# Optimization experiments

Measured on AMD Instinct MI355X. Metric: run time of the kernel, lower is better.

Reference implementation:

```python
import jax, jax.numpy as jnp
import numpy as np

WS = 7          # window_size
NH = 12         # num_heads
EPS = 1e-5      # LayerNorm eps


def setup_inputs() -> dict:
    key = jax.random.key(0)
    ks = jax.random.split(key, 8)
    B, H, W, C = 32, 56, 56, 384
    x = jax.random.normal(ks[0], (B, H * W, C), dtype=jnp.float32)
    s = 1.0 / np.sqrt(C)
    return {
        "x": x,
        "ln_gamma": jnp.ones((C,), jnp.float32),
        "ln_beta": jnp.zeros((C,), jnp.float32),
        "w_in": jax.random.normal(ks[1], (3 * C, C), jnp.float32) * s,   # torch in_proj_weight
        "b_in": jnp.zeros((3 * C,), jnp.float32),
        "w_out": jax.random.normal(ks[2], (C, C), jnp.float32) * s,      # torch out_proj.weight
        "b_out": jnp.zeros((C,), jnp.float32),
        "H": H,
        "W": W,
    }


def reference(x, ln_gamma, ln_beta, w_in, b_in, w_out, b_out, H, W):
    B, N, C = x.shape
    assert N == H * W
    hd = C // NH
    shortcut = x

    # LayerNorm
    mu = jnp.mean(x, axis=-1, keepdims=True)
    var = jnp.mean((x - mu) ** 2, axis=-1, keepdims=True)
    y = (x - mu) * jax.lax.rsqrt(var + EPS) * ln_gamma + ln_beta

    # window partition (pads are static Python ints)
    y = y.reshape(B, H, W, C)
    pad_h = (WS - H % WS) % WS
    pad_w = (WS - W % WS) % WS
    y = jnp.pad(y, ((0, 0), (0, pad_h), (0, pad_w), (0, 0)))
    Hp, Wp = H + pad_h, W + pad_w
    nh, nw = Hp // WS, Wp // WS
    y = y.reshape(B, nh, WS, nw, WS, C).transpose(0, 1, 3, 2, 4, 5)
    y = y.reshape(B * nh * nw, WS * WS, C)   # [NWIN, L, C]

    # MHA (torch nn.MultiheadAttention, batch_first)
    qkv = y @ w_in.T + b_in                   # [NWIN, L, 3C]
    q, k, v = jnp.split(qkv, 3, axis=-1)
    NWIN, L, _ = y.shape
    q = q.reshape(NWIN, L, NH, hd).transpose(0, 2, 1, 3)
    k = k.reshape(NWIN, L, NH, hd).transpose(0, 2, 1, 3)
    v = v.reshape(NWIN, L, NH, hd).transpose(0, 2, 1, 3)
    scores = jnp.einsum("whqd,whkd->whqk", q, k) / jnp.sqrt(jnp.float32(hd))
    attn = jax.nn.softmax(scores, axis=-1)
    o = jnp.einsum("whqk,whkd->whqd", attn, v)
    o = o.transpose(0, 2, 1, 3).reshape(NWIN, L, C)
    o = o @ w_out.T + b_out

    # window reverse + unpad + residual
    o = o.reshape(B, nh, nw, WS, WS, C).transpose(0, 1, 3, 2, 4, 5)
    o = o.reshape(B, Hp, Wp, C)[:, :H, :W, :].reshape(B, N, C)
    return shortcut + o
```

## Files before the change

kernel.cpp:

```cpp
#include <hip/hip_runtime.h>

typedef __bf16 bf16x8 __attribute__((ext_vector_type(8)));
typedef float f32x4 __attribute__((ext_vector_type(4)));
typedef unsigned short ushort8 __attribute__((ext_vector_type(8)));
typedef unsigned int uu2 __attribute__((ext_vector_type(2)));

#define LDS_AS(p) ((__attribute__((address_space(3))) void*)(p))
#define GLB_AS(p) ((const __attribute__((address_space(1))) void*)(p))

__device__ __forceinline__ unsigned short f2bf(float f) {
    union { float f; unsigned u; } v; v.f = f;
    unsigned r = v.u + 0x7fffu + ((v.u >> 16) & 1u);
    return (unsigned short)(r >> 16);
}

__global__ __launch_bounds__(256) void convw_kernel(
    const float* __restrict__ wi, const float* __restrict__ wo,
    unsigned short* __restrict__ qw, unsigned short* __restrict__ ow)
{
    const int i = blockIdx.x * 256 + threadIdx.x;
    if (i < 1152 * 384) qw[i] = f2bf(wi[i]);
    if (i < 384 * 384)  ow[i] = f2bf(wo[i]);
}

__global__ __launch_bounds__(256) void ln_kernel(
    const float* __restrict__ x, const float* __restrict__ gam,
    const float* __restrict__ bet, unsigned short* __restrict__ y)
{
    const int lane = threadIdx.x & 63;
    const int wv   = threadIdx.x >> 6;
    const int m    = blockIdx.x * 4 + wv;
    const int win  = m / 49, l = m - win * 49;
    const int b = win >> 6, wh = (win >> 3) & 7, ww = win & 7;
    const int i = l / 7, j = l - i * 7;
    const float2* xr = (const float2*)(x + ((size_t)b * 3136 + (wh * 7 + i) * 56 + (ww * 7 + j)) * 384);

    float2 v[3];
    float s = 0.f, ss = 0.f;
#pragma unroll
    for (int t = 0; t < 3; ++t) {
        v[t] = xr[t * 64 + lane];
        s  += v[t].x + v[t].y;
        ss += v[t].x * v[t].x + v[t].y * v[t].y;
    }
#pragma unroll
    for (int d = 1; d < 64; d <<= 1) {
        s  += __shfl_xor(s, d, 64);
        ss += __shfl_xor(ss, d, 64);
    }
    const float mu  = s * (1.f / 384.f);
    const float var = ss * (1.f / 384.f) - mu * mu;
    const float rs  = rsqrtf(var + 1e-5f);

    unsigned* yr = (unsigned*)(y + (size_t)m * 384);
#pragma unroll
    for (int t = 0; t < 3; ++t) {
        const int c = (t * 64 + lane) * 2;
        float a0 = (v[t].x - mu) * rs * gam[c]     + bet[c];
        float a1 = (v[t].y - mu) * rs * gam[c + 1] + bet[c + 1];
        yr[t * 64 + lane] = (unsigned)f2bf(a0) | ((unsigned)f2bf(a1) << 16);
    }
}

template <int N_, int EPI>
__global__ __launch_bounds__(256) void gemm_kernel(
    const unsigned short* __restrict__ A,
    const unsigned short* __restrict__ Bw,
    const float* __restrict__ bias,
    unsigned short* __restrict__ obf,
    const float* __restrict__ xres,
    float* __restrict__ oflt)
{
    __shared__ unsigned short As[3][128 * 32];
    __shared__ unsigned short Bs[3][128 * 32];
    const int lane = threadIdx.x & 63;
    const int wv   = threadIdx.x >> 6;

    const int NB = N_ / 128;
    int sw = blockIdx.x;
    if ((gridDim.x & 7) == 0)
        sw = (sw & 7) * (int)(gridDim.x >> 3) + (sw >> 3);
    const int my = sw / NB;
    const int m0 = my * 128;
    const int n0 = (sw - my * NB) * 128;

    const int wm = (wv & 1) * 64;
    const int wn = (wv >> 1) * 64;
    const int cl = lane & 15;
    const int qd = lane >> 4;
    const int srow = wv * 16 + (lane >> 2);
    const int scol = ((lane & 3) ^ ((lane >> 3) & 3)) * 8;
    const int rc   = (qd ^ ((cl >> 1) & 3)) * 8;

    const unsigned short* gA = A  + (size_t)(m0 + srow) * 384 + scol;
    const unsigned short* gB = Bw + (size_t)(n0 + srow) * 384 + scol;

    f32x4 acc[4][4] = {};

#define STAGE(BUF, KB) do {                                                                                   \
    __builtin_amdgcn_global_load_lds(GLB_AS(gA + (KB) * 32),            LDS_AS(&As[BUF][(wv * 16) * 32]),      16, 0, 0); \
    __builtin_amdgcn_global_load_lds(GLB_AS(gA + 64 * 384 + (KB) * 32), LDS_AS(&As[BUF][(64 + wv * 16) * 32]), 16, 0, 0); \
    __builtin_amdgcn_global_load_lds(GLB_AS(gB + (KB) * 32),            LDS_AS(&Bs[BUF][(wv * 16) * 32]),      16, 0, 0); \
    __builtin_amdgcn_global_load_lds(GLB_AS(gB + 64 * 384 + (KB) * 32), LDS_AS(&Bs[BUF][(64 + wv * 16) * 32]), 16, 0, 0); \
  } while (0)

    STAGE(0, 0);
    STAGE(1, 1);

#pragma unroll
    for (int kb = 0; kb < 12; ++kb) {
        const int cur = kb % 3;
        if (kb < 11) asm volatile("s_waitcnt vmcnt(4)\n\ts_barrier" ::: "memory");
        else         asm volatile("s_waitcnt vmcnt(0)\n\ts_barrier" ::: "memory");

        if (kb < 10) STAGE((kb + 2) % 3, kb + 2);

        bf16x8 af[4], bfr[4];
#pragma unroll
        for (int mt = 0; mt < 4; ++mt)
            af[mt] = *(const bf16x8*)(&As[cur][(wm + mt * 16 + cl) * 32 + rc]);
#pragma unroll
        for (int nt = 0; nt < 4; ++nt)
            bfr[nt] = *(const bf16x8*)(&Bs[cur][(wn + nt * 16 + cl) * 32 + rc]);
#pragma unroll
        for (int mt = 0; mt < 4; ++mt)
#pragma unroll
            for (int nt = 0; nt < 4; ++nt)
                acc[mt][nt] = __builtin_amdgcn_mfma_f32_16x16x32_bf16(bfr[nt], af[mt], acc[mt][nt], 0, 0, 0);
    }
#undef STAGE

#pragma unroll
    for (int mt = 0; mt < 4; ++mt) {
        const int m = m0 + wm + mt * 16 + cl;
        size_t rowbase = 0;
        if (EPI == 1) {
            const int win = m / 49, l = m - win * 49;
            const int b = win >> 6, wh = (win >> 3) & 7, ww = win & 7;
            const int i = l / 7, j = l - i * 7;
            rowbase = ((size_t)b * 3136 + (wh * 7 + i) * 56 + (ww * 7 + j)) * 384;
        }
#pragma unroll
        for (int nt = 0; nt < 4; ++nt) {
            const int nb = n0 + wn + nt * 16 + qd * 4;
            const f32x4 bv = *(const f32x4*)(bias + nb);
            if (EPI == 0) {
                uu2 p;
                p[0] = (unsigned)f2bf(acc[mt][nt][0] + bv[0]) |
                       ((unsigned)f2bf(acc[mt][nt][1] + bv[1]) << 16);
                p[1] = (unsigned)f2bf(acc[mt][nt][2] + bv[2]) |
                       ((unsigned)f2bf(acc[mt][nt][3] + bv[3]) << 16);
                *(uu2*)(obf + (size_t)m * N_ + nb) = p;
            } else {
                const f32x4 xr = *(const f32x4*)(xres + rowbase + nb);
                f32x4 o;
#pragma unroll
                for (int r = 0; r < 4; ++r) o[r] = acc[mt][nt][r] + bv[r] + xr[r];
                *(f32x4*)(oflt + rowbase + nb) = o;
            }
        }
    }
}

__global__ __launch_bounds__(256) void attn_kernel(
    const unsigned short* __restrict__ qkv, unsigned short* __restrict__ o)
{
    __shared__ unsigned short P[4][64 * 72];
    const int lane = threadIdx.x & 63;
    const int wv   = threadIdx.x >> 6;
    const int cl = lane & 15;
    const int qd = lane >> 4;
    const int g   = blockIdx.x * 4 + wv;
    const int win = g / 12;
    const int h   = g - win * 12;
    const unsigned short* base = qkv + (size_t)win * (49 * 1152);

    bf16x8 aq[4], bk[4];
#pragma unroll
    for (int mt = 0; mt < 4; ++mt) {
        const int l = mt * 16 + cl;
        bf16x8 z = {};
        if (l < 49) z = *(const bf16x8*)(base + (size_t)l * 1152 + h * 32 + qd * 8);
        aq[mt] = z;
    }
#pragma unroll
    for (int nt = 0; nt < 4; ++nt) {
        const int lk = nt * 16 + cl;
        bf16x8 z = {};
        if (lk < 49) z = *(const bf16x8*)(base + (size_t)lk * 1152 + 384 + h * 32 + qd * 8);
        bk[nt] = z;
    }
    f32x4 s[4][4] = {};
#pragma unroll
    for (int mt = 0; mt < 4; ++mt)
#pragma unroll
        for (int nt = 0; nt < 4; ++nt)
            s[mt][nt] = __builtin_amdgcn_mfma_f32_16x16x32_bf16(aq[mt], bk[nt], s[mt][nt], 0, 0, 0);

    const float scale = 0.17677669529663687f;
#pragma unroll
    for (int mt = 0; mt < 4; ++mt)
#pragma unroll
        for (int nt = 0; nt < 4; ++nt)
#pragma unroll
            for (int r = 0; r < 4; ++r) {
                float t = s[mt][nt][r] * scale;
                if (nt * 16 + cl >= 49) t = -1e30f;
                s[mt][nt][r] = t;
            }

#pragma unroll
    for (int mt = 0; mt < 4; ++mt)
#pragma unroll
        for (int r = 0; r < 4; ++r) {
            float mx = fmaxf(fmaxf(s[mt][0][r], s[mt][1][r]), fmaxf(s[mt][2][r], s[mt][3][r]));
            mx = fmaxf(mx, __shfl_xor(mx, 1, 64));
            mx = fmaxf(mx, __shfl_xor(mx, 2, 64));
            mx = fmaxf(mx, __shfl_xor(mx, 4, 64));
            mx = fmaxf(mx, __shfl_xor(mx, 8, 64));
            float sm = 0.f;
#pragma unroll
            for (int nt = 0; nt < 4; ++nt) {
                const float p = __expf(s[mt][nt][r] - mx);
                s[mt][nt][r] = p;
                sm += p;
            }
            sm += __shfl_xor(sm, 1, 64);
            sm += __shfl_xor(sm, 2, 64);
            sm += __shfl_xor(sm, 4, 64);
            sm += __shfl_xor(sm, 8, 64);
            const float inv = 1.f / sm;
#pragma unroll
            for (int nt = 0; nt < 4; ++nt)
                s[mt][nt][r] *= inv;
        }

    unsigned short* Pw = &P[wv][0];
#pragma unroll
    for (int mt = 0; mt < 4; ++mt)
#pragma unroll
        for (int nt = 0; nt < 4; ++nt)
#pragma unroll
            for (int r = 0; r < 4; ++r)
                Pw[(mt * 16 + qd * 4 + r) * 72 + nt * 16 + cl] = f2bf(s[mt][nt][r]);

    f32x4 oa[4][2] = {};
    const unsigned short* vbase = base + 768 + h * 32;
#pragma unroll
    for (int kk = 0; kk < 2; ++kk) {
        bf16x8 ap[4];
#pragma unroll
        for (int mt = 0; mt < 4; ++mt)
            ap[mt] = *(const bf16x8*)(Pw + (mt * 16 + cl) * 72 + kk * 32 + qd * 8);
#pragma unroll
        for (int nt = 0; nt < 2; ++nt) {
            ushort8 tv;
#pragma unroll
            for (int jj = 0; jj < 8; ++jj) {
                const int lk = kk * 32 + qd * 8 + jj;
                tv[jj] = (lk < 49) ? vbase[(size_t)lk * 1152 + nt * 16 + cl] : (unsigned short)0;
            }
            const bf16x8 bv = __builtin_bit_cast(bf16x8, tv);
#pragma unroll
            for (int mt = 0; mt < 4; ++mt)
                oa[mt][nt] = __builtin_amdgcn_mfma_f32_16x16x32_bf16(ap[mt], bv, oa[mt][nt], 0, 0, 0);
        }
    }

    unsigned short* ob = o + (size_t)win * 49 * 384 + h * 32;
#pragma unroll
    for (int mt = 0; mt < 4; ++mt)
#pragma unroll
        for (int r = 0; r < 4; ++r) {
            const int l = mt * 16 + qd * 4 + r;
            if (l < 49) {
#pragma unroll
                for (int nt = 0; nt < 2; ++nt)
                    ob[(size_t)l * 384 + nt * 16 + cl] = f2bf(oa[mt][nt][r]);
            }
        }
}

extern "C" void kernel_launch(void* const* d_in, const int* in_sizes, int n_in,
                              void* d_out, int out_size, void* d_ws, size_t ws_size,
                              hipStream_t stream)
{
    const float* x   = (const float*)d_in[0];
    const float* gam = (const float*)d_in[1];
    const float* bet = (const float*)d_in[2];
    const float* wi  = (const float*)d_in[3];
    const float* bi  = (const float*)d_in[4];
    const float* wo  = (const float*)d_in[5];
    const float* bo  = (const float*)d_in[6];
    float* out = (float*)d_out;

    const int Bb   = in_sizes[0] / (3136 * 384);
    const int M    = Bb * 3136;
    const int NWIN = Bb * 64;

    char* ws = (char*)d_ws;
    unsigned short* qw   = (unsigned short*)(ws);
    unsigned short* ow   = (unsigned short*)(ws + 884736);
    unsigned short* y    = (unsigned short*)(ws + 1179648);
    unsigned short* qkv  = (unsigned short*)(ws + 1179648 + (size_t)M * 768);
    unsigned short* owin = (unsigned short*)(ws + 1179648 + (size_t)M * 768 + (size_t)M * 2304);

    convw_kernel<<<1728, 256, 0, stream>>>(wi, wo, qw, ow);
    ln_kernel<<<M / 4, 256, 0, stream>>>(x, gam, bet, y);
    gemm_kernel<1152, 0><<<(M / 128) * 9, 256, 0, stream>>>(y, qw, bi, qkv, nullptr, nullptr);
    attn_kernel<<<NWIN * 12 / 4, 256, 0, stream>>>(qkv, owin);
    gemm_kernel<384, 1><<<(M / 128) * 3, 256, 0, stream>>>(owin, ow, bo, nullptr, x, out);
}
```

Measured before the change: 641.9 us.

## Write V transposed per window-head and enlarge GEMM tiles to 256x128

The QKV GEMM epilogue now writes the V part into a per-(window, head) transposed, zero-padded buffer, so the attention kernel can load V fragments with single vector loads instead of strided scalar gathers. The GEMM tile grows to 256 rows with 512 threads, which reuses each B tile across more rows. The attention output now reuses the LayerNorm buffer. The costs are scattered 2-byte stores in the GEMM epilogue, extra zero-fill work in the weight-convert kernel, and higher LDS and register use per block, which may lower occupancy.

```diff
diff --git a/kernel.cpp b/kernel.cpp
--- a/kernel.cpp
+++ b/kernel.cpp
@@ -16,11 +16,17 @@
 
 __global__ __launch_bounds__(256) void convw_kernel(
     const float* __restrict__ wi, const float* __restrict__ wo,
-    unsigned short* __restrict__ qw, unsigned short* __restrict__ ow)
+    unsigned short* __restrict__ qw, unsigned short* __restrict__ ow,
+    unsigned short* __restrict__ vt)
 {
     const int i = blockIdx.x * 256 + threadIdx.x;
     if (i < 1152 * 384) qw[i] = f2bf(wi[i]);
     if (i < 384 * 384)  ow[i] = f2bf(wo[i]);
+    if (i < 786432) {
+        unsigned short* p = vt + (size_t)i * 64;
+#pragma unroll
+        for (int c = 49; c < 64; ++c) p[c] = 0;
+    }
 }
 
 __global__ __launch_bounds__(256) void ln_kernel(
@@ -63,15 +69,16 @@
 }
 
 template <int N_, int EPI>
-__global__ __launch_bounds__(256) void gemm_kernel(
+__global__ __launch_bounds__(512, 4) void gemm_kernel(
     const unsigned short* __restrict__ A,
     const unsigned short* __restrict__ Bw,
     const float* __restrict__ bias,
     unsigned short* __restrict__ obf,
+    unsigned short* __restrict__ vt,
     const float* __restrict__ xres,
     float* __restrict__ oflt)
 {
-    __shared__ unsigned short As[3][128 * 32];
+    __shared__ unsigned short As[3][256 * 32];
     __shared__ unsigned short Bs[3][128 * 32];
     const int lane = threadIdx.x & 63;
     const int wv   = threadIdx.x >> 6;
@@ -81,27 +88,26 @@
     if ((gridDim.x & 7) == 0)
         sw = (sw & 7) * (int)(gridDim.x >> 3) + (sw >> 3);
     const int my = sw / NB;
-    const int m0 = my * 128;
+    const int m0 = my * 256;
     const int n0 = (sw - my * NB) * 128;
 
-    const int wm = (wv & 1) * 64;
-    const int wn = (wv >> 1) * 64;
+    const int wm = (wv & 3) * 64;
+    const int wn = (wv >> 2) * 64;
     const int cl = lane & 15;
     const int qd = lane >> 4;
-    const int srow = wv * 16 + (lane >> 2);
+    const int srow = lane >> 2;
     const int scol = ((lane & 3) ^ ((lane >> 3) & 3)) * 8;
     const int rc   = (qd ^ ((cl >> 1) & 3)) * 8;
 
-    const unsigned short* gA = A  + (size_t)(m0 + srow) * 384 + scol;
-    const unsigned short* gB = Bw + (size_t)(n0 + srow) * 384 + scol;
+    const unsigned short* gA = A  + (size_t)(m0 + wv * 32 + srow) * 384 + scol;
+    const unsigned short* gB = Bw + (size_t)(n0 + wv * 16 + srow) * 384 + scol;
 
     f32x4 acc[4][4] = {};
 
-#define STAGE(BUF, KB) do {                                                                                   \
-    __builtin_amdgcn_global_load_lds(GLB_AS(gA + (KB) * 32),            LDS_AS(&As[BUF][(wv * 16) * 32]),      16, 0, 0); \
-    __builtin_amdgcn_global_load_lds(GLB_AS(gA + 64 * 384 + (KB) * 32), LDS_AS(&As[BUF][(64 + wv * 16) * 32]), 16, 0, 0); \
+#define STAGE(BUF, KB) do {                                                                                        \
+    __builtin_amdgcn_global_load_lds(GLB_AS(gA + (KB) * 32),            LDS_AS(&As[BUF][(wv * 32) * 32]),      16, 0, 0); \
+    __builtin_amdgcn_global_load_lds(GLB_AS(gA + 16 * 384 + (KB) * 32), LDS_AS(&As[BUF][(wv * 32 + 16) * 32]), 16, 0, 0); \
     __builtin_amdgcn_global_load_lds(GLB_AS(gB + (KB) * 32),            LDS_AS(&Bs[BUF][(wv * 16) * 32]),      16, 0, 0); \
-    __builtin_amdgcn_global_load_lds(GLB_AS(gB + 64 * 384 + (KB) * 32), LDS_AS(&Bs[BUF][(64 + wv * 16) * 32]), 16, 0, 0); \
   } while (0)
 
     STAGE(0, 0);
@@ -110,7 +116,7 @@
 #pragma unroll
     for (int kb = 0; kb < 12; ++kb) {
         const int cur = kb % 3;
-        if (kb < 11) asm volatile("s_waitcnt vmcnt(4)\n\ts_barrier" ::: "memory");
+        if (kb < 11) asm volatile("s_waitcnt vmcnt(3)\n\ts_barrier" ::: "memory");
         else         asm volatile("s_waitcnt vmcnt(0)\n\ts_barrier" ::: "memory");
 
         if (kb < 10) STAGE((kb + 2) % 3, kb + 2);
@@ -133,9 +139,9 @@
 #pragma unroll
     for (int mt = 0; mt < 4; ++mt) {
         const int m = m0 + wm + mt * 16 + cl;
+        const int win = m / 49, l = m - win * 49;
         size_t rowbase = 0;
         if (EPI == 1) {
-            const int win = m / 49, l = m - win * 49;
             const int b = win >> 6, wh = (win >> 3) & 7, ww = win & 7;
             const int i = l / 7, j = l - i * 7;
             rowbase = ((size_t)b * 3136 + (wh * 7 + i) * 56 + (ww * 7 + j)) * 384;
@@ -145,12 +151,21 @@
             const int nb = n0 + wn + nt * 16 + qd * 4;
             const f32x4 bv = *(const f32x4*)(bias + nb);
             if (EPI == 0) {
-                uu2 p;
-                p[0] = (unsigned)f2bf(acc[mt][nt][0] + bv[0]) |
-                       ((unsigned)f2bf(acc[mt][nt][1] + bv[1]) << 16);
-                p[1] = (unsigned)f2bf(acc[mt][nt][2] + bv[2]) |
-                       ((unsigned)f2bf(acc[mt][nt][3] + bv[3]) << 16);
-                *(uu2*)(obf + (size_t)m * N_ + nb) = p;
+                if (n0 < 768) {
+                    uu2 p;
+                    p[0] = (unsigned)f2bf(acc[mt][nt][0] + bv[0]) |
+                           ((unsigned)f2bf(acc[mt][nt][1] + bv[1]) << 16);
+                    p[1] = (unsigned)f2bf(acc[mt][nt][2] + bv[2]) |
+                           ((unsigned)f2bf(acc[mt][nt][3] + bv[3]) << 16);
+                    *(uu2*)(obf + (size_t)m * 768 + nb) = p;
+                } else {
+                    const int cf = nb - 768;
+                    const int h = cf >> 5, c0 = cf & 31;
+                    unsigned short* vp = vt + ((size_t)(win * 12 + h) * 32 + c0) * 64 + l;
+#pragma unroll
+                    for (int r = 0; r < 4; ++r)
+                        vp[r * 64] = f2bf(acc[mt][nt][r] + bv[r]);
+                }
             } else {
                 const f32x4 xr = *(const f32x4*)(xres + rowbase + nb);
                 f32x4 o;
@@ -163,7 +178,9 @@
 }
 
 __global__ __launch_bounds__(256) void attn_kernel(
-    const unsigned short* __restrict__ qkv, unsigned short* __restrict__ o)
+    const unsigned short* __restrict__ qkv,
+    const unsigned short* __restrict__ vt,
+    unsigned short* __restrict__ o)
 {
     __shared__ unsigned short P[4][64 * 72];
     const int lane = threadIdx.x & 63;
@@ -173,21 +190,21 @@
     const int g   = blockIdx.x * 4 + wv;
     const int win = g / 12;
     const int h   = g - win * 12;
-    const unsigned short* base = qkv + (size_t)win * (49 * 1152);
+    const unsigned short* base = qkv + (size_t)win * (49 * 768);
 
     bf16x8 aq[4], bk[4];
 #pragma unroll
     for (int mt = 0; mt < 4; ++mt) {
         const int l = mt * 16 + cl;
         bf16x8 z = {};
-        if (l < 49) z = *(const bf16x8*)(base + (size_t)l * 1152 + h * 32 + qd * 8);
+        if (l < 49) z = *(const bf16x8*)(base + (size_t)l * 768 + h * 32 + qd * 8);
         aq[mt] = z;
     }
 #pragma unroll
     for (int nt = 0; nt < 4; ++nt) {
         const int lk = nt * 16 + cl;
         bf16x8 z = {};
-        if (lk < 49) z = *(const bf16x8*)(base + (size_t)lk * 1152 + 384 + h * 32 + qd * 8);
+        if (lk < 49) z = *(const bf16x8*)(base + (size_t)lk * 768 + 384 + h * 32 + qd * 8);
         bk[nt] = z;
     }
     f32x4 s[4][4] = {};
@@ -245,7 +262,7 @@
                 Pw[(mt * 16 + qd * 4 + r) * 72 + nt * 16 + cl] = f2bf(s[mt][nt][r]);
 
     f32x4 oa[4][2] = {};
-    const unsigned short* vbase = base + 768 + h * 32;
+    const unsigned short* vtb = vt + (size_t)(win * 12 + h) * 2048;
 #pragma unroll
     for (int kk = 0; kk < 2; ++kk) {
         bf16x8 ap[4];
@@ -254,13 +271,7 @@
             ap[mt] = *(const bf16x8*)(Pw + (mt * 16 + cl) * 72 + kk * 32 + qd * 8);
 #pragma unroll
         for (int nt = 0; nt < 2; ++nt) {
-            ushort8 tv;
-#pragma unroll
-            for (int jj = 0; jj < 8; ++jj) {
-                const int lk = kk * 32 + qd * 8 + jj;
-                tv[jj] = (lk < 49) ? vbase[(size_t)lk * 1152 + nt * 16 + cl] : (unsigned short)0;
-            }
-            const bf16x8 bv = __builtin_bit_cast(bf16x8, tv);
+            const bf16x8 bv = *(const bf16x8*)(vtb + (size_t)(nt * 16 + cl) * 64 + kk * 32 + qd * 8);
 #pragma unroll
             for (int mt = 0; mt < 4; ++mt)
                 oa[mt][nt] = __builtin_amdgcn_mfma_f32_16x16x32_bf16(ap[mt], bv, oa[mt][nt], 0, 0, 0);
@@ -303,11 +314,12 @@
     unsigned short* ow   = (unsigned short*)(ws + 884736);
     unsigned short* y    = (unsigned short*)(ws + 1179648);
     unsigned short* qkv  = (unsigned short*)(ws + 1179648 + (size_t)M * 768);
-    unsigned short* owin = (unsigned short*)(ws + 1179648 + (size_t)M * 768 + (size_t)M * 2304);
-
-    convw_kernel<<<1728, 256, 0, stream>>>(wi, wo, qw, ow);
+    unsigned short* vt   = (unsigned short*)(ws + 1179648 + (size_t)M * 768 + (size_t)M * 1536);
+    unsigned short* owin = y;
+
+    convw_kernel<<<3072, 256, 0, stream>>>(wi, wo, qw, ow, vt);
     ln_kernel<<<M / 4, 256, 0, stream>>>(x, gam, bet, y);
-    gemm_kernel<1152, 0><<<(M / 128) * 9, 256, 0, stream>>>(y, qw, bi, qkv, nullptr, nullptr);
-    attn_kernel<<<NWIN * 12 / 4, 256, 0, stream>>>(qkv, owin);
-    gemm_kernel<384, 1><<<(M / 128) * 3, 256, 0, stream>>>(owin, ow, bo, nullptr, x, out);
-}
+    gemm_kernel<1152, 0><<<(M / 256) * 9, 512, 0, stream>>>(y, qw, bi, qkv, vt, nullptr, nullptr);
+    attn_kernel<<<NWIN * 12 / 4, 256, 0, stream>>>(qkv, vt, owin);
+    gemm_kernel<384, 1><<<(M / 256) * 3, 512, 0, stream>>>(owin, ow, bo, nullptr, nullptr, x, out);
+}
```

Result: slower. 691.1 us (+7.7%).

## Fuse window attention with output projection and residual per window

Applied to the files above, without the earlier changes.

Attention and the output projection are merged into one kernel with one block per window. Each wave handles three heads and writes its bf16 head outputs into a shared LDS tile. The block then multiplies that tile by w_out, read directly from global memory without LDS staging, and adds bias and the residual. This removes the owin intermediate round trip and one kernel launch. In exchange, every block re-reads the full w_out from cache, the projection is done in 49-row tiles with lower MFMA efficiency, and LDS use is larger, which may lower occupancy.

```diff
diff --git a/kernel.cpp b/kernel.cpp
--- a/kernel.cpp
+++ b/kernel.cpp
@@ -62,21 +62,18 @@
     }
 }
 
-template <int N_, int EPI>
-__global__ __launch_bounds__(256) void gemm_kernel(
+__global__ __launch_bounds__(256) void gemm_qkv_kernel(
     const unsigned short* __restrict__ A,
     const unsigned short* __restrict__ Bw,
     const float* __restrict__ bias,
-    unsigned short* __restrict__ obf,
-    const float* __restrict__ xres,
-    float* __restrict__ oflt)
+    unsigned short* __restrict__ obf)
 {
     __shared__ unsigned short As[3][128 * 32];
     __shared__ unsigned short Bs[3][128 * 32];
     const int lane = threadIdx.x & 63;
     const int wv   = threadIdx.x >> 6;
 
-    const int NB = N_ / 128;
+    const int NB = 9;
     int sw = blockIdx.x;
     if ((gridDim.x & 7) == 0)
         sw = (sw & 7) * (int)(gridDim.x >> 3) + (sw >> 3);
@@ -133,152 +130,185 @@
 #pragma unroll
     for (int mt = 0; mt < 4; ++mt) {
         const int m = m0 + wm + mt * 16 + cl;
-        size_t rowbase = 0;
-        if (EPI == 1) {
-            const int win = m / 49, l = m - win * 49;
-            const int b = win >> 6, wh = (win >> 3) & 7, ww = win & 7;
-            const int i = l / 7, j = l - i * 7;
-            rowbase = ((size_t)b * 3136 + (wh * 7 + i) * 56 + (ww * 7 + j)) * 384;
-        }
 #pragma unroll
         for (int nt = 0; nt < 4; ++nt) {
             const int nb = n0 + wn + nt * 16 + qd * 4;
             const f32x4 bv = *(const f32x4*)(bias + nb);
-            if (EPI == 0) {
-                uu2 p;
-                p[0] = (unsigned)f2bf(acc[mt][nt][0] + bv[0]) |
-                       ((unsigned)f2bf(acc[mt][nt][1] + bv[1]) << 16);
-                p[1] = (unsigned)f2bf(acc[mt][nt][2] + bv[2]) |
-                       ((unsigned)f2bf(acc[mt][nt][3] + bv[3]) << 16);
-                *(uu2*)(obf + (size_t)m * N_ + nb) = p;
-            } else {
-                const f32x4 xr = *(const f32x4*)(xres + rowbase + nb);
-                f32x4 o;
-#pragma unroll
-                for (int r = 0; r < 4; ++r) o[r] = acc[mt][nt][r] + bv[r] + xr[r];
-                *(f32x4*)(oflt + rowbase + nb) = o;
-            }
-        }
-    }
-}
-
-__global__ __launch_bounds__(256) void attn_kernel(
-    const unsigned short* __restrict__ qkv, unsigned short* __restrict__ o)
-{
+            uu2 p;
+            p[0] = (unsigned)f2bf(acc[mt][nt][0] + bv[0]) |
+                   ((unsigned)f2bf(acc[mt][nt][1] + bv[1]) << 16);
+            p[1] = (unsigned)f2bf(acc[mt][nt][2] + bv[2]) |
+                   ((unsigned)f2bf(acc[mt][nt][3] + bv[3]) << 16);
+            *(uu2*)(obf + (size_t)m * 1152 + nb) = p;
+        }
+    }
+}
+
+#define OT_STRIDE 392
+__global__ __launch_bounds__(256) void attn_out_kernel(
+    const unsigned short* __restrict__ qkv,
+    const unsigned short* __restrict__ wout,
+    const float* __restrict__ bias,
+    const float* __restrict__ xres,
+    float* __restrict__ out)
+{
+    __shared__ unsigned short OT[49 * OT_STRIDE];
     __shared__ unsigned short P[4][64 * 72];
     const int lane = threadIdx.x & 63;
     const int wv   = threadIdx.x >> 6;
     const int cl = lane & 15;
     const int qd = lane >> 4;
-    const int g   = blockIdx.x * 4 + wv;
-    const int win = g / 12;
-    const int h   = g - win * 12;
+    const int win = blockIdx.x;
     const unsigned short* base = qkv + (size_t)win * (49 * 1152);
-
-    bf16x8 aq[4], bk[4];
+    unsigned short* Pw = &P[wv][0];
+
+    for (int rep = 0; rep < 3; ++rep) {
+        const int h = wv * 3 + rep;
+
+        bf16x8 aq[4], bk[4];
+#pragma unroll
+        for (int mt = 0; mt < 4; ++mt) {
+            const int l = mt * 16 + cl;
+            bf16x8 z = {};
+            if (l < 49) z = *(const bf16x8*)(base + (size_t)l * 1152 + h * 32 + qd * 8);
+            aq[mt] = z;
+        }
+#pragma unroll
+        for (int nt = 0; nt < 4; ++nt) {
+            const int lk = nt * 16 + cl;
+            bf16x8 z = {};
+            if (lk < 49) z = *(const bf16x8*)(base + (size_t)lk * 1152 + 384 + h * 32 + qd * 8);
+            bk[nt] = z;
+        }
+        f32x4 s[4][4] = {};
+#pragma unroll
+        for (int mt = 0; mt < 4; ++mt)
+#pragma unroll
+            for (int nt = 0; nt < 4; ++nt)
+                s[mt][nt] = __builtin_amdgcn_mfma_f32_16x16x32_bf16(aq[mt], bk[nt], s[mt][nt], 0, 0, 0);
+
+        const float scale = 0.17677669529663687f;
+#pragma unroll
+        for (int mt = 0; mt < 4; ++mt)
+#pragma unroll
+            for (int nt = 0; nt < 4; ++nt)
+#pragma unroll
+                for (int r = 0; r < 4; ++r) {
+                    float t = s[mt][nt][r] * scale;
+                    if (nt * 16 + cl >= 49) t = -1e30f;
+                    s[mt][nt][r] = t;
+                }
+
+#pragma unroll
+        for (int mt = 0; mt < 4; ++mt)
+#pragma unroll
+            for (int r = 0; r < 4; ++r) {
+                float mx = fmaxf(fmaxf(s[mt][0][r], s[mt][1][r]), fmaxf(s[mt][2][r], s[mt][3][r]));
+                mx = fmaxf(mx, __shfl_xor(mx, 1, 64));
+                mx = fmaxf(mx, __shfl_xor(mx, 2, 64));
+                mx = fmaxf(mx, __shfl_xor(mx, 4, 64));
+                mx = fmaxf(mx, __shfl_xor(mx, 8, 64));
+                float sm = 0.f;
+#pragma unroll
+                for (int nt = 0; nt < 4; ++nt) {
+                    const float p = __expf(s[mt][nt][r] - mx);
+                    s[mt][nt][r] = p;
+                    sm += p;
+                }
+                sm += __shfl_xor(sm, 1, 64);
+                sm += __shfl_xor(sm, 2, 64);
+                sm += __shfl_xor(sm, 4, 64);
+                sm += __shfl_xor(sm, 8, 64);
+                const float inv = 1.f / sm;
+#pragma unroll
+                for (int nt = 0; nt < 4; ++nt)
+                    s[mt][nt][r] *= inv;
+            }
+
+#pragma unroll
+        for (int mt = 0; mt < 4; ++mt)
+#pragma unroll
+            for (int nt = 0; nt < 4; ++nt)
+#pragma unroll
+                for (int r = 0; r < 4; ++r)
+                    Pw[(mt * 16 + qd * 4 + r) * 72 + nt * 16 + cl] = f2bf(s[mt][nt][r]);
+
+        f32x4 oa[4][2] = {};
+        const unsigned short* vbase = base + 768 + h * 32;
+#pragma unroll
+        for (int kk = 0; kk < 2; ++kk) {
+            bf16x8 ap[4];
+#pragma unroll
+            for (int mt = 0; mt < 4; ++mt)
+                ap[mt] = *(const bf16x8*)(Pw + (mt * 16 + cl) * 72 + kk * 32 + qd * 8);
+#pragma unroll
+            for (int nt = 0; nt < 2; ++nt) {
+                ushort8 tv;
+#pragma unroll
+                for (int jj = 0; jj < 8; ++jj) {
+                    const int lk = kk * 32 + qd * 8 + jj;
+                    tv[jj] = (lk < 49) ? vbase[(size_t)lk * 1152 + nt * 16 + cl] : (unsigned short)0;
+                }
+                const bf16x8 bv = __builtin_bit_cast(bf16x8, tv);
+#pragma unroll
+                for (int mt = 0; mt < 4; ++mt)
+                    oa[mt][nt] = __builtin_amdgcn_mfma_f32_16x16x32_bf16(ap[mt], bv, oa[mt][nt], 0, 0, 0);
+            }
+        }
+
+#pragma unroll
+        for (int mt = 0; mt < 4; ++mt)
+#pragma unroll
+            for (int r = 0; r < 4; ++r) {
+                const int l = mt * 16 + qd * 4 + r;
+                if (l < 49) {
+#pragma unroll
+                    for (int nt = 0; nt < 2; ++nt)
+                        OT[l * OT_STRIDE + h * 32 + nt * 16 + cl] = f2bf(oa[mt][nt][r]);
+                }
+            }
+    }
+
+    __syncthreads();
+
+    const int nbase = wv * 96;
+    f32x4 acc[4][6] = {};
+#pragma unroll
+    for (int kb = 0; kb < 12; ++kb) {
+        const int k0 = kb * 32;
+        bf16x8 af[4], bw[6];
+#pragma unroll
+        for (int mt = 0; mt < 4; ++mt)
+            af[mt] = *(const bf16x8*)(OT + (mt * 16 + cl) * OT_STRIDE + k0 + qd * 8);
+#pragma unroll
+        for (int nt = 0; nt < 6; ++nt)
+            bw[nt] = *(const bf16x8*)(wout + (size_t)(nbase + nt * 16 + cl) * 384 + k0 + qd * 8);
+#pragma unroll
+        for (int mt = 0; mt < 4; ++mt)
+#pragma unroll
+            for (int nt = 0; nt < 6; ++nt)
+                acc[mt][nt] = __builtin_amdgcn_mfma_f32_16x16x32_bf16(bw[nt], af[mt], acc[mt][nt], 0, 0, 0);
+    }
+
+    const int b = win >> 6, wh = (win >> 3) & 7, ww = win & 7;
 #pragma unroll
     for (int mt = 0; mt < 4; ++mt) {
         const int l = mt * 16 + cl;
-        bf16x8 z = {};
-        if (l < 49) z = *(const bf16x8*)(base + (size_t)l * 1152 + h * 32 + qd * 8);
-        aq[mt] = z;
-    }
-#pragma unroll
-    for (int nt = 0; nt < 4; ++nt) {
-        const int lk = nt * 16 + cl;
-        bf16x8 z = {};
-        if (lk < 49) z = *(const bf16x8*)(base + (size_t)lk * 1152 + 384 + h * 32 + qd * 8);
-        bk[nt] = z;
-    }
-    f32x4 s[4][4] = {};
-#pragma unroll
-    for (int mt = 0; mt < 4; ++mt)
-#pragma unroll
-        for (int nt = 0; nt < 4; ++nt)
-            s[mt][nt] = __builtin_amdgcn_mfma_f32_16x16x32_bf16(aq[mt], bk[nt], s[mt][nt], 0, 0, 0);
-
-    const float scale = 0.17677669529663687f;
-#pragma unroll
-    for (int mt = 0; mt < 4; ++mt)
-#pragma unroll
-        for (int nt = 0; nt < 4; ++nt)
-#pragma unroll
-            for (int r = 0; r < 4; ++r) {
-                float t = s[mt][nt][r] * scale;
-                if (nt * 16 + cl >= 49) t = -1e30f;
-                s[mt][nt][r] = t;
+        if (l < 49) {
+            const int i = l / 7, j = l - i * 7;
+            const size_t rowbase = ((size_t)b * 3136 + (wh * 7 + i) * 56 + (ww * 7 + j)) * 384;
+#pragma unroll
+            for (int nt = 0; nt < 6; ++nt) {
+                const int n = nbase + nt * 16 + qd * 4;
+                const f32x4 bv = *(const f32x4*)(bias + n);
+                const f32x4 xr = *(const f32x4*)(xres + rowbase + n);
+                f32x4 o;
+#pragma unroll
+                for (int r = 0; r < 4; ++r) o[r] = acc[mt][nt][r] + bv[r] + xr[r];
+                *(f32x4*)(out + rowbase + n) = o;
             }
-
-#pragma unroll
-    for (int mt = 0; mt < 4; ++mt)
-#pragma unroll
-        for (int r = 0; r < 4; ++r) {
-            float mx = fmaxf(fmaxf(s[mt][0][r], s[mt][1][r]), fmaxf(s[mt][2][r], s[mt][3][r]));
-            mx = fmaxf(mx, __shfl_xor(mx, 1, 64));
-            mx = fmaxf(mx, __shfl_xor(mx, 2, 64));
-            mx = fmaxf(mx, __shfl_xor(mx, 4, 64));
-            mx = fmaxf(mx, __shfl_xor(mx, 8, 64));
-            float sm = 0.f;
-#pragma unroll
-            for (int nt = 0; nt < 4; ++nt) {
-                const float p = __expf(s[mt][nt][r] - mx);
-                s[mt][nt][r] = p;
-                sm += p;
-            }
-            sm += __shfl_xor(sm, 1, 64);
-            sm += __shfl_xor(sm, 2, 64);
-            sm += __shfl_xor(sm, 4, 64);
-            sm += __shfl_xor(sm, 8, 64);
-            const float inv = 1.f / sm;
-#pragma unroll
-            for (int nt = 0; nt < 4; ++nt)
-                s[mt][nt][r] *= inv;
-        }
-
-    unsigned short* Pw = &P[wv][0];
-#pragma unroll
-    for (int mt = 0; mt < 4; ++mt)
-#pragma unroll
-        for (int nt = 0; nt < 4; ++nt)
-#pragma unroll
-            for (int r = 0; r < 4; ++r)
-                Pw[(mt * 16 + qd * 4 + r) * 72 + nt * 16 + cl] = f2bf(s[mt][nt][r]);
-
-    f32x4 oa[4][2] = {};
-    const unsigned short* vbase = base + 768 + h * 32;
-#pragma unroll
-    for (int kk = 0; kk < 2; ++kk) {
-        bf16x8 ap[4];
-#pragma unroll
-        for (int mt = 0; mt < 4; ++mt)
-            ap[mt] = *(const bf16x8*)(Pw + (mt * 16 + cl) * 72 + kk * 32 + qd * 8);
-#pragma unroll
-        for (int nt = 0; nt < 2; ++nt) {
-            ushort8 tv;
-#pragma unroll
-            for (int jj = 0; jj < 8; ++jj) {
-                const int lk = kk * 32 + qd * 8 + jj;
-                tv[jj] = (lk < 49) ? vbase[(size_t)lk * 1152 + nt * 16 + cl] : (unsigned short)0;
-            }
-            const bf16x8 bv = __builtin_bit_cast(bf16x8, tv);
-#pragma unroll
-            for (int mt = 0; mt < 4; ++mt)
-                oa[mt][nt] = __builtin_amdgcn_mfma_f32_16x16x32_bf16(ap[mt], bv, oa[mt][nt], 0, 0, 0);
-        }
-    }
-
-    unsigned short* ob = o + (size_t)win * 49 * 384 + h * 32;
-#pragma unroll
-    for (int mt = 0; mt < 4; ++mt)
-#pragma unroll
-        for (int r = 0; r < 4; ++r) {
-            const int l = mt * 16 + qd * 4 + r;
-            if (l < 49) {
-#pragma unroll
-                for (int nt = 0; nt < 2; ++nt)
-                    ob[(size_t)l * 384 + nt * 16 + cl] = f2bf(oa[mt][nt][r]);
-            }
-        }
+        }
+    }
 }
 
 extern "C" void kernel_launch(void* const* d_in, const int* in_sizes, int n_in,
@@ -303,11 +333,9 @@
     unsigned short* ow   = (unsigned short*)(ws + 884736);
     unsigned short* y    = (unsigned short*)(ws + 1179648);
     unsigned short* qkv  = (unsigned short*)(ws + 1179648 + (size_t)M * 768);
-    unsigned short* owin = (unsigned short*)(ws + 1179648 + (size_t)M * 768 + (size_t)M * 2304);
 
     convw_kernel<<<1728, 256, 0, stream>>>(wi, wo, qw, ow);
     ln_kernel<<<M / 4, 256, 0, stream>>>(x, gam, bet, y);
-    gemm_kernel<1152, 0><<<(M / 128) * 9, 256, 0, stream>>>(y, qw, bi, qkv, nullptr, nullptr);
-    attn_kernel<<<NWIN * 12 / 4, 256, 0, stream>>>(qkv, owin);
-    gemm_kernel<384, 1><<<(M / 128) * 3, 256, 0, stream>>>(owin, ow, bo, nullptr, x, out);
-}
+    gemm_qkv_kernel<<<(M / 128) * 9, 256, 0, stream>>>(y, qw, bi, qkv);
+    attn_out_kernel<<<NWIN, 256, 0, stream>>>(qkv, ow, bo, x, out);
+}
```

After: 731.7 us. 14.0% more time.
